# Optimization experiments

Measured on AMD Instinct MI355X. Metric: run time of the kernel, lower is better.

The kernel has to match this reference:

```python
import jax, jax.numpy as jnp
import numpy as np

CUTOFF = 5.0       # module __init__ arg
BOX_L = 40.0       # side of cubic region positions are drawn from (OBC: no box passed)
N_ATOMS = 8192
MAX_PAIRS = 1_048_576  # static bound on directed pairs (expected ~550k)


def setup_inputs() -> dict:
    key = jax.random.key(0)
    positions = jax.random.uniform(key, (N_ATOMS, 3), dtype=jnp.float32) * BOX_L
    return {"positions": positions}


def _pairwise_dist(x):
    # Euclidean distance matrix via the gram trick (avoids [N,N,3] intermediate).
    sq = jnp.sum(x * x, axis=1)
    d2 = sq[:, None] + sq[None, :] - 2.0 * (x @ x.T)
    return jnp.sqrt(jnp.maximum(d2, 0.0))


def _safe_norm(dr):
    # norm with zero-safe gradient (padded pairs have dr == 0)
    d2 = jnp.sum(dr * dr, axis=1)
    ok = d2 > 0
    return jnp.where(ok, jnp.sqrt(jnp.where(ok, d2, 1.0)), 0.0)


def reference(positions):
    n = positions.shape[0]
    dist = _pairwise_dist(positions)                      # [N, N]
    mask = (dist < CUTOFF) & (~jnp.eye(n, dtype=bool))    # exclude self-pairs
    # torch.argwhere equivalent, padded to static size; padding -> (0, 0)
    i, j = jnp.nonzero(mask, size=MAX_PAIRS, fill_value=0)
    pairs = jnp.stack([i, j], axis=1).astype(jnp.int32)   # [MAX_PAIRS, 2]
    # pairs_buffer_scales: 1 where i < j else 0 (padding (0,0) -> 0)
    buffer_scales = (i < j).astype(jnp.int32)
    # pairs_ds (pbc_flag=False): ||r_j - r_i||
    dr = positions[j] - positions[i]                      # [MAX_PAIRS, 3]
    ds = _safe_norm(dr)
    return pairs, buffer_scales, ds
```

## Files before the change

kernel.cpp:

```cpp
#include <hip/hip_runtime.h>

#define MAXP 1048576
#define NATOMS 8192
#define D2_CUT 0x1.8ffffep+4f
#define CINV 0.175f
#define CAP 192

#define S_BASE    (3 * MAXP + 524288)
#define S_CELLCNT (S_BASE)
#define S_CELLOFF (S_BASE + 512)
#define S_CURSOR  (S_BASE + 1024)
#define S_ROWCNT  (S_BASE + 2048)
#define S_ROWOFF  (S_BASE + 10240)
#define S_SORTID  (S_BASE + 18432)
#define S_SORTPOS (S_BASE + 32768)
#define S_END     (S_BASE + 65536)
#define IDX_LIMIT 524288

__device__ __forceinline__ float sq3_nc(float x, float y, float z) {
#pragma clang fp contract(off)
  float a = x * x;
  float b = y * y;
  float c = z * z;
  return (a + b) + c;
}

__device__ __forceinline__ float d2_gram(float xi, float yi, float zi, float sqi,
                                         float xj, float yj, float zj, float sqj) {
#pragma clang fp contract(off)
  float g = xi * xj;
  g = __builtin_fmaf(yi, yj, g);
  g = __builtin_fmaf(zi, zj, g);
  float t = sqi + sqj;
  float d2 = t - 2.0f * g;
  return d2;
}

__device__ __forceinline__ float d2_direct(float xi, float yi, float zi,
                                           float xj, float yj, float zj) {
#pragma clang fp contract(off)
  float dx = xj - xi;
  float dy = yj - yi;
  float dz = zj - zi;
  float a = dx * dx;
  float b = dy * dy;
  float c = dz * dz;
  return (a + b) + c;
}

__device__ __forceinline__ int cellco(float v) {
  int c = (int)(v * CINV);
  return c < 0 ? 0 : (c > 6 ? 6 : c);
}

__global__ __launch_bounds__(256) void nl_fill(float4* __restrict__ out) {
  out[blockIdx.x * 256 + threadIdx.x] = make_float4(0.f, 0.f, 0.f, 0.f);
}

__global__ __launch_bounds__(256) void nl_bin(const float* __restrict__ pos,
                                              float* __restrict__ out) {
  int* cellcnt = (int*)(out + S_CELLCNT);
  int a = blockIdx.x * 256 + threadIdx.x;
  float x = pos[3 * a], y = pos[3 * a + 1], z = pos[3 * a + 2];
  int c = cellco(x) + 7 * cellco(y) + 49 * cellco(z);
  atomicAdd(&cellcnt[c], 1);
}

__global__ __launch_bounds__(512) void nl_binscan(float* __restrict__ out) {
  const int* cellcnt = (const int*)(out + S_CELLCNT);
  int* celloff = (int*)(out + S_CELLOFF);
  __shared__ int s[512];
  int tid = threadIdx.x;
  s[tid] = (tid < 343) ? cellcnt[tid] : 0;
  __syncthreads();
  for (int off = 1; off < 512; off <<= 1) {
    int v = (tid >= off) ? s[tid - off] : 0;
    __syncthreads();
    s[tid] += v;
    __syncthreads();
  }
  if (tid < 344) celloff[tid] = (tid == 0) ? 0 : s[tid - 1];
}

__global__ __launch_bounds__(256) void nl_scatter(const float* __restrict__ pos,
                                                  float* __restrict__ out) {
  const int* celloff = (const int*)(out + S_CELLOFF);
  int* cursor = (int*)(out + S_CURSOR);
  int* sortid = (int*)(out + S_SORTID);
  float4* sortpos = (float4*)(out + S_SORTPOS);
  int a = blockIdx.x * 256 + threadIdx.x;
  float x = pos[3 * a], y = pos[3 * a + 1], z = pos[3 * a + 2];
  int c = cellco(x) + 7 * cellco(y) + 49 * cellco(z);
  int slot = celloff[c] + atomicAdd(&cursor[c], 1);
  sortid[slot] = a;
  sortpos[slot] = make_float4(x, y, z, sq3_nc(x, y, z));
}

__global__ __launch_bounds__(256) void nl_rowcount(const float* __restrict__ pos,
                                                   float* __restrict__ out) {
  const int* celloff = (const int*)(out + S_CELLOFF);
  const int* sortid = (const int*)(out + S_SORTID);
  const float4* sortpos = (const float4*)(out + S_SORTPOS);
  int* rowcnt = (int*)(out + S_ROWCNT);
  const int lane = threadIdx.x & 63;
  const int wave = threadIdx.x >> 6;
  const int row = blockIdx.x * 4 + wave;
  float xi = pos[3 * row], yi = pos[3 * row + 1], zi = pos[3 * row + 2];
  float sqi = sq3_nc(xi, yi, zi);
  int cx = cellco(xi), cy = cellco(yi), cz = cellco(zi);
  int x0 = max(cx - 1, 0), x1 = min(cx + 1, 6);
  int y0 = max(cy - 1, 0), y1 = min(cy + 1, 6);
  int z0 = max(cz - 1, 0), z1 = min(cz + 1, 6);
  int cnt = 0;
  for (int icz = z0; icz <= z1; ++icz)
    for (int icy = y0; icy <= y1; ++icy) {
      int cb = 7 * icy + 49 * icz;
      int s = celloff[cb + x0];
      int e = celloff[cb + x1 + 1];
      for (int b = s; b < e; b += 64) {
        int t = b + lane;
        bool v = t < e;
        float4 p = v ? sortpos[t] : make_float4(1e30f, 1e30f, 1e30f, 0.f);
        int j = v ? sortid[t] : -1;
        float d2 = d2_gram(xi, yi, zi, sqi, p.x, p.y, p.z, p.w);
        cnt += (v && (d2 < D2_CUT) && (j != row)) ? 1 : 0;
      }
    }
  for (int off = 32; off > 0; off >>= 1) cnt += __shfl_down(cnt, off, 64);
  if (lane == 0) rowcnt[row] = cnt;
}

__global__ __launch_bounds__(1024) void nl_rowscan(float* __restrict__ out) {
  const int* cnts = (const int*)(out + S_ROWCNT);
  int* offs = (int*)(out + S_ROWOFF);
  __shared__ int s[1024];
  const int tid = threadIdx.x;
  const int base = tid * 8;
  int local[8];
  int sum = 0;
#pragma unroll
  for (int k = 0; k < 8; ++k) { local[k] = sum; sum += cnts[base + k]; }
  s[tid] = sum;
  __syncthreads();
  for (int off = 1; off < 1024; off <<= 1) {
    int v = (tid >= off) ? s[tid - off] : 0;
    __syncthreads();
    s[tid] += v;
    __syncthreads();
  }
  int excl = (tid == 0) ? 0 : s[tid - 1];
#pragma unroll
  for (int k = 0; k < 8; ++k) offs[base + k] = excl + local[k];
}

__global__ __launch_bounds__(256) void nl_rowwrite(const float* __restrict__ pos,
                                                   float* __restrict__ out) {
  const int* celloff = (const int*)(out + S_CELLOFF);
  const int* sortid = (const int*)(out + S_SORTID);
  const float4* sortpos = (const float4*)(out + S_SORTPOS);
  const int* rowoff = (const int*)(out + S_ROWOFF);
  __shared__ int jb[4][CAP];
  __shared__ float db[4][CAP];
  const int lane = threadIdx.x & 63;
  const int wave = threadIdx.x >> 6;
  const int row = blockIdx.x * 4 + wave;
  float xi = pos[3 * row], yi = pos[3 * row + 1], zi = pos[3 * row + 2];
  float sqi = sq3_nc(xi, yi, zi);
  int cx = cellco(xi), cy = cellco(yi), cz = cellco(zi);
  int x0 = max(cx - 1, 0), x1 = min(cx + 1, 6);
  int y0 = max(cy - 1, 0), y1 = min(cy + 1, 6);
  int z0 = max(cz - 1, 0), z1 = min(cz + 1, 6);
  int cnt = 0;
  for (int icz = z0; icz <= z1; ++icz)
    for (int icy = y0; icy <= y1; ++icy) {
      int cb = 7 * icy + 49 * icz;
      int s = celloff[cb + x0];
      int e = celloff[cb + x1 + 1];
      for (int b = s; b < e; b += 64) {
        int t = b + lane;
        bool v = t < e;
        float4 p = v ? sortpos[t] : make_float4(1e30f, 1e30f, 1e30f, 0.f);
        int j = v ? sortid[t] : -1;
        float d2 = d2_gram(xi, yi, zi, sqi, p.x, p.y, p.z, p.w);
        bool pred = v && (d2 < D2_CUT) && (j != row);
        unsigned long long m = __ballot(pred ? 1 : 0);
        if (pred) {
          int ps = cnt + __popcll(m & ((1ull << lane) - 1ull));
          if (ps < CAP) {
            jb[wave][ps] = j;
            db[wave][ps] = sqrtf(d2_direct(xi, yi, zi, p.x, p.y, p.z));
          }
        }
        cnt += __popcll(m);
      }
    }
  __syncthreads();
  int k = cnt > CAP ? CAP : cnt;
  int base = rowoff[row];
  for (int midx = lane; midx < k; midx += 64) {
    int jm = jb[wave][midx];
    int rank = 0;
    for (int t = 0; t < k; ++t) rank += (jb[wave][t] < jm) ? 1 : 0;
    int idx = base + rank;
    if (idx < IDX_LIMIT) {
      ((float2*)out)[idx] = make_float2((float)row, (float)jm);
      out[2 * MAXP + idx] = (row < jm) ? 1.0f : 0.0f;
      out[3 * MAXP + idx] = db[wave][midx];
    }
  }
}

__global__ __launch_bounds__(256) void nl_padstage(float4* __restrict__ tail) {
  tail[blockIdx.x * 256 + threadIdx.x] = make_float4(0.f, 0.f, 0.f, 0.f);
}

extern "C" void kernel_launch(void* const* d_in, const int* in_sizes, int n_in,
                              void* d_out, int out_size, void* d_ws, size_t ws_size,
                              hipStream_t stream) {
  const float* pos = (const float*)d_in[0];
  float* out = (float*)d_out;

  nl_fill<<<MAXP / 256, 256, 0, stream>>>((float4*)out);
  nl_bin<<<NATOMS / 256, 256, 0, stream>>>(pos, out);
  nl_binscan<<<1, 512, 0, stream>>>(out);
  nl_scatter<<<NATOMS / 256, 256, 0, stream>>>(pos, out);
  nl_rowcount<<<NATOMS / 4, 256, 0, stream>>>(pos, out);
  nl_rowscan<<<1, 1024, 0, stream>>>(out);
  nl_rowwrite<<<NATOMS / 4, 256, 0, stream>>>(pos, out);
  nl_padstage<<<64, 256, 0, stream>>>((float4*)(out + S_BASE));
}
```

Before: 102.6 us.

## Fuse neighbor-list stages into three kernels and move scratch into workspace

Result: slower. 109.8 us (+7.0%).

```diff
diff --git a/kernel.cpp b/kernel.cpp
--- a/kernel.cpp
+++ b/kernel.cpp
@@ -6,16 +6,10 @@
 #define CINV 0.175f
 #define CAP 192
 
-#define S_BASE    (3 * MAXP + 524288)
-#define S_CELLCNT (S_BASE)
-#define S_CELLOFF (S_BASE + 512)
-#define S_CURSOR  (S_BASE + 1024)
-#define S_ROWCNT  (S_BASE + 2048)
-#define S_ROWOFF  (S_BASE + 10240)
-#define S_SORTID  (S_BASE + 18432)
-#define S_SORTPOS (S_BASE + 32768)
-#define S_END     (S_BASE + 65536)
-#define IDX_LIMIT 524288
+#define W_CELLOFF 0
+#define W_SORTID  512
+#define W_SORTPOS 16384
+#define W_ROWCNT  49152
 
 __device__ __forceinline__ float sq3_nc(float x, float y, float z) {
 #pragma clang fp contract(off)
@@ -53,58 +47,65 @@
   return c < 0 ? 0 : (c > 6 ? 6 : c);
 }
 
-__global__ __launch_bounds__(256) void nl_fill(float4* __restrict__ out) {
-  out[blockIdx.x * 256 + threadIdx.x] = make_float4(0.f, 0.f, 0.f, 0.f);
-}
-
-__global__ __launch_bounds__(256) void nl_bin(const float* __restrict__ pos,
-                                              float* __restrict__ out) {
-  int* cellcnt = (int*)(out + S_CELLCNT);
-  int a = blockIdx.x * 256 + threadIdx.x;
-  float x = pos[3 * a], y = pos[3 * a + 1], z = pos[3 * a + 2];
-  int c = cellco(x) + 7 * cellco(y) + 49 * cellco(z);
-  atomicAdd(&cellcnt[c], 1);
-}
-
-__global__ __launch_bounds__(512) void nl_binscan(float* __restrict__ out) {
-  const int* cellcnt = (const int*)(out + S_CELLCNT);
-  int* celloff = (int*)(out + S_CELLOFF);
+__global__ __launch_bounds__(1024) void nl_bin(const float* __restrict__ pos,
+                                               float* __restrict__ ws) {
+  __shared__ int hcnt[343];
+  __shared__ int hoff[344];
+  __shared__ int hcur[343];
   __shared__ int s[512];
-  int tid = threadIdx.x;
-  s[tid] = (tid < 343) ? cellcnt[tid] : 0;
+  const int tid = threadIdx.x;
+  if (tid < 343) { hcnt[tid] = 0; hcur[tid] = 0; }
+  __syncthreads();
+
+  float x[8], y[8], z[8];
+  int cl[8];
+#pragma unroll
+  for (int k = 0; k < 8; ++k) {
+    int a = tid + k * 1024;
+    x[k] = pos[3 * a]; y[k] = pos[3 * a + 1]; z[k] = pos[3 * a + 2];
+    cl[k] = cellco(x[k]) + 7 * cellco(y[k]) + 49 * cellco(z[k]);
+    atomicAdd(&hcnt[cl[k]], 1);
+  }
+  __syncthreads();
+
+  if (tid < 512) s[tid] = (tid < 343) ? hcnt[tid] : 0;
   __syncthreads();
   for (int off = 1; off < 512; off <<= 1) {
-    int v = (tid >= off) ? s[tid - off] : 0;
-    __syncthreads();
-    s[tid] += v;
-    __syncthreads();
-  }
-  if (tid < 344) celloff[tid] = (tid == 0) ? 0 : s[tid - 1];
-}
-
-__global__ __launch_bounds__(256) void nl_scatter(const float* __restrict__ pos,
-                                                  float* __restrict__ out) {
-  const int* celloff = (const int*)(out + S_CELLOFF);
-  int* cursor = (int*)(out + S_CURSOR);
-  int* sortid = (int*)(out + S_SORTID);
-  float4* sortpos = (float4*)(out + S_SORTPOS);
-  int a = blockIdx.x * 256 + threadIdx.x;
-  float x = pos[3 * a], y = pos[3 * a + 1], z = pos[3 * a + 2];
-  int c = cellco(x) + 7 * cellco(y) + 49 * cellco(z);
-  int slot = celloff[c] + atomicAdd(&cursor[c], 1);
-  sortid[slot] = a;
-  sortpos[slot] = make_float4(x, y, z, sq3_nc(x, y, z));
-}
-
-__global__ __launch_bounds__(256) void nl_rowcount(const float* __restrict__ pos,
-                                                   float* __restrict__ out) {
-  const int* celloff = (const int*)(out + S_CELLOFF);
-  const int* sortid = (const int*)(out + S_SORTID);
-  const float4* sortpos = (const float4*)(out + S_SORTPOS);
-  int* rowcnt = (int*)(out + S_ROWCNT);
+    int v = (tid < 512 && tid >= off) ? s[tid - off] : 0;
+    __syncthreads();
+    if (tid < 512) s[tid] += v;
+    __syncthreads();
+  }
+  if (tid < 343) hoff[tid] = (tid == 0) ? 0 : s[tid - 1];
+  if (tid == 343) hoff[343] = NATOMS;
+  __syncthreads();
+  if (tid < 344) ((int*)(ws + W_CELLOFF))[tid] = hoff[tid];
+
+  int* sortid = (int*)(ws + W_SORTID);
+  float4* sortpos = (float4*)(ws + W_SORTPOS);
+#pragma unroll
+  for (int k = 0; k < 8; ++k) {
+    int slot = hoff[cl[k]] + atomicAdd(&hcur[cl[k]], 1);
+    sortid[slot] = tid + k * 1024;
+    sortpos[slot] = make_float4(x[k], y[k], z[k], sq3_nc(x[k], y[k], z[k]));
+  }
+}
+
+__global__ __launch_bounds__(256) void nl_count_fill(const float* __restrict__ pos,
+                                                     float* __restrict__ out,
+                                                     float* __restrict__ ws) {
+  float4* o4 = (float4*)out;
+  const int b = blockIdx.x;
+  o4[b * 512 + threadIdx.x] = make_float4(0.f, 0.f, 0.f, 0.f);
+  o4[b * 512 + 256 + threadIdx.x] = make_float4(0.f, 0.f, 0.f, 0.f);
+
+  const int* celloff = (const int*)(ws + W_CELLOFF);
+  const int* sortid = (const int*)(ws + W_SORTID);
+  const float4* sortpos = (const float4*)(ws + W_SORTPOS);
+  int* rowcnt = (int*)(ws + W_ROWCNT);
   const int lane = threadIdx.x & 63;
   const int wave = threadIdx.x >> 6;
-  const int row = blockIdx.x * 4 + wave;
+  const int row = b * 4 + wave;
   float xi = pos[3 * row], yi = pos[3 * row + 1], zi = pos[3 * row + 2];
   float sqi = sq3_nc(xi, yi, zi);
   int cx = cellco(xi), cy = cellco(yi), cz = cellco(zi);
@@ -117,8 +118,8 @@
       int cb = 7 * icy + 49 * icz;
       int s = celloff[cb + x0];
       int e = celloff[cb + x1 + 1];
-      for (int b = s; b < e; b += 64) {
-        int t = b + lane;
+      for (int bb = s; bb < e; bb += 64) {
+        int t = bb + lane;
         bool v = t < e;
         float4 p = v ? sortpos[t] : make_float4(1e30f, 1e30f, 1e30f, 0.f);
         int j = v ? sortid[t] : -1;
@@ -130,40 +131,36 @@
   if (lane == 0) rowcnt[row] = cnt;
 }
 
-__global__ __launch_bounds__(1024) void nl_rowscan(float* __restrict__ out) {
-  const int* cnts = (const int*)(out + S_ROWCNT);
-  int* offs = (int*)(out + S_ROWOFF);
-  __shared__ int s[1024];
-  const int tid = threadIdx.x;
-  const int base = tid * 8;
-  int local[8];
-  int sum = 0;
-#pragma unroll
-  for (int k = 0; k < 8; ++k) { local[k] = sum; sum += cnts[base + k]; }
-  s[tid] = sum;
-  __syncthreads();
-  for (int off = 1; off < 1024; off <<= 1) {
-    int v = (tid >= off) ? s[tid - off] : 0;
-    __syncthreads();
-    s[tid] += v;
-    __syncthreads();
-  }
-  int excl = (tid == 0) ? 0 : s[tid - 1];
-#pragma unroll
-  for (int k = 0; k < 8; ++k) offs[base + k] = excl + local[k];
-}
-
-__global__ __launch_bounds__(256) void nl_rowwrite(const float* __restrict__ pos,
-                                                   float* __restrict__ out) {
-  const int* celloff = (const int*)(out + S_CELLOFF);
-  const int* sortid = (const int*)(out + S_SORTID);
-  const float4* sortpos = (const float4*)(out + S_SORTPOS);
-  const int* rowoff = (const int*)(out + S_ROWOFF);
+__global__ __launch_bounds__(256) void nl_write(const float* __restrict__ pos,
+                                                float* __restrict__ out,
+                                                const float* __restrict__ ws) {
+  const int* celloff = (const int*)(ws + W_CELLOFF);
+  const int* sortid = (const int*)(ws + W_SORTID);
+  const float4* sortpos = (const float4*)(ws + W_SORTPOS);
+  const int* rowcnt = (const int*)(ws + W_ROWCNT);
+  __shared__ int pfx[NATOMS];
+  __shared__ int tsum[256];
   __shared__ int jb[4][CAP];
   __shared__ float db[4][CAP];
-  const int lane = threadIdx.x & 63;
-  const int wave = threadIdx.x >> 6;
+  const int tid = threadIdx.x;
+  const int lane = tid & 63;
+  const int wave = tid >> 6;
   const int row = blockIdx.x * 4 + wave;
+
+  int run = 0;
+  for (int k = 0; k < 32; ++k) {
+    pfx[tid * 32 + k] = run;
+    run += rowcnt[tid * 32 + k];
+  }
+  tsum[tid] = run;
+  __syncthreads();
+  for (int off = 1; off < 256; off <<= 1) {
+    int v = (tid >= off) ? tsum[tid - off] : 0;
+    __syncthreads();
+    tsum[tid] += v;
+    __syncthreads();
+  }
+
   float xi = pos[3 * row], yi = pos[3 * row + 1], zi = pos[3 * row + 2];
   float sqi = sq3_nc(xi, yi, zi);
   int cx = cellco(xi), cy = cellco(yi), cz = cellco(zi);
@@ -176,8 +173,8 @@
       int cb = 7 * icy + 49 * icz;
       int s = celloff[cb + x0];
       int e = celloff[cb + x1 + 1];
-      for (int b = s; b < e; b += 64) {
-        int t = b + lane;
+      for (int bb = s; bb < e; bb += 64) {
+        int t = bb + lane;
         bool v = t < e;
         float4 p = v ? sortpos[t] : make_float4(1e30f, 1e30f, 1e30f, 0.f);
         int j = v ? sortid[t] : -1;
@@ -195,23 +192,20 @@
       }
     }
   __syncthreads();
+
   int k = cnt > CAP ? CAP : cnt;
-  int base = rowoff[row];
+  int base = pfx[row] + ((row >= 32) ? tsum[(row >> 5) - 1] : 0);
   for (int midx = lane; midx < k; midx += 64) {
     int jm = jb[wave][midx];
     int rank = 0;
     for (int t = 0; t < k; ++t) rank += (jb[wave][t] < jm) ? 1 : 0;
     int idx = base + rank;
-    if (idx < IDX_LIMIT) {
+    if (idx < MAXP) {
       ((float2*)out)[idx] = make_float2((float)row, (float)jm);
       out[2 * MAXP + idx] = (row < jm) ? 1.0f : 0.0f;
       out[3 * MAXP + idx] = db[wave][midx];
     }
   }
-}
-
-__global__ __launch_bounds__(256) void nl_padstage(float4* __restrict__ tail) {
-  tail[blockIdx.x * 256 + threadIdx.x] = make_float4(0.f, 0.f, 0.f, 0.f);
 }
 
 extern "C" void kernel_launch(void* const* d_in, const int* in_sizes, int n_in,
@@ -219,13 +213,9 @@
                               hipStream_t stream) {
   const float* pos = (const float*)d_in[0];
   float* out = (float*)d_out;
-
-  nl_fill<<<MAXP / 256, 256, 0, stream>>>((float4*)out);
-  nl_bin<<<NATOMS / 256, 256, 0, stream>>>(pos, out);
-  nl_binscan<<<1, 512, 0, stream>>>(out);
-  nl_scatter<<<NATOMS / 256, 256, 0, stream>>>(pos, out);
-  nl_rowcount<<<NATOMS / 4, 256, 0, stream>>>(pos, out);
-  nl_rowscan<<<1, 1024, 0, stream>>>(out);
-  nl_rowwrite<<<NATOMS / 4, 256, 0, stream>>>(pos, out);
-  nl_padstage<<<64, 256, 0, stream>>>((float4*)(out + S_BASE));
-}
+  float* ws = (float*)d_ws;
+
+  nl_bin<<<1, 1024, 0, stream>>>(pos, ws);
+  nl_count_fill<<<2048, 256, 0, stream>>>(pos, out, ws);
+  nl_write<<<2048, 256, 0, stream>>>(pos, out, ws);
+}
```
